# Kernel tuning notes

Measured on AMD Instinct MI355X. Metric: run time of the kernel, lower is better.

Reference implementation:

```python
import jax, jax.numpy as jnp
import numpy as np


def setup_inputs() -> dict:
    key = jax.random.key(0)
    ks = jax.random.split(key, 16)
    B, S, H = 512, 128, 256
    f32 = jnp.float32
    inputs = jax.random.normal(ks[0], (B, S, 2), f32)
    # xavier-normal-ish init (gain/sqrt(fan_in+fan_out) approximated by small scale)
    def xn(k, shape):
        fan = shape[0] + shape[1]
        return jax.random.normal(k, shape, f32) * np.sqrt(2.0 / fan)
    return {
        "inputs": inputs,
        "W0": xn(ks[1], (H, 2)),   "b0": jnp.zeros((H,), f32),
        "W1": xn(ks[2], (H, H)),   "b1": jnp.zeros((H,), f32),
        "W2": xn(ks[3], (H, H)),   "b2": jnp.zeros((H,), f32),
        "W3": xn(ks[4], (H, H)),   "b3": jnp.zeros((H,), f32),
        "W4": xn(ks[5], (1, H)),   "b4": jnp.zeros((1,), f32),
        "log_growth_rate": jax.random.normal(ks[6], (), f32),
        "log_carrying_capacity": jax.random.normal(ks[7], (), f32),
        "log_initial_loss": jax.random.normal(ks[8], (), f32),
        "in_mean": jnp.array([0.5, 50.0], f32),
        "in_std": jnp.array([0.2, 30.0], f32),
        "tgt_mean": jnp.array([0.8], f32),
        "tgt_std": jnp.array([0.1], f32),
    }


def reference(inputs, W0, b0, W1, b1, W2, b2, W3, b3, W4, b4,
              log_growth_rate, log_carrying_capacity, log_initial_loss,
              in_mean, in_std, tgt_mean, tgt_std):
    B, S = inputs.shape[0], inputs.shape[1]
    # PDE parameters (Verhulst logistic growth)
    r = jnp.exp(-log_growth_rate)
    K = 0.2 + (1.0 - 0.2) * jax.nn.sigmoid(log_carrying_capacity)  # carrying capacity in [0.2, 1]
    C = 0.0 + (0.1 - 0.0) * jax.nn.sigmoid(log_initial_loss)       # initial loss in [0, 0.1]

    # split state feature s and time t, standardize per-column
    s = inputs[..., 0:1].reshape(-1, 1)  # [N,1]
    t = inputs[..., 1:2].reshape(-1, 1)  # [N,1]
    s_norm = (s - in_mean[0:1]) / (in_std[0:1] + 1e-8)
    t_norm = (t - in_mean[1:2]) / (in_std[1:2] + 1e-8)

    Ws = (W0, W1, W2, W3, W4)
    bs = (b0, b1, b2, b3, b4)

    def mlp(x):  # [N,2] -> [N,1], tanh MLP
        h = x
        for W, b in zip(Ws[:-1], bs[:-1]):
            h = jnp.tanh(h @ W.T + b)
        return h @ Ws[-1].T + bs[-1]

    def u_of(tn):  # U(s_norm, tn), inverse-standardized targets
        return mlp(jnp.concatenate([s_norm, tn], axis=-1)) * tgt_std + tgt_mean

    ones = jnp.ones_like(t_norm)

    def uf_of(tn):
        # U and U_t = dU/dt_norm (forward-mode; each point depends on its own scalar t)
        U, U_dot = jax.jvp(u_of, (tn,), (ones,))
        U_t = U_dot.sum(-1, keepdims=True)
        G = r * (U - C) * (1.0 - (U - C) / (K - C))  # Verhulst
        return U, U_t - G  # (U, F)

    # second derivative w.r.t. t_norm: F_t = U_tt - G_t
    (U, F), (_, F_t) = jax.jvp(uf_of, (t_norm,), (ones,))

    shp = (B, S, 1)
    return U.reshape(shp), F.reshape(shp), F_t.reshape(shp)
```

## Files before the change

kernel.cpp:

```cpp
#include <hip/hip_runtime.h>
#include <hip/hip_bf16.h>
#include <math.h>

typedef short s8v __attribute__((ext_vector_type(8)));
typedef float f4v __attribute__((ext_vector_type(4)));

#define HH 256
#define TP 32
#define NTHREADS 256
#define KSTR 520
#define TSTR 4160
#define NTILES 6
#define PLANE (NTILES * TSTR)

__device__ __forceinline__ unsigned short bf_rne(float x){
    union{float f;unsigned u;}v; v.f=x;
    unsigned r = v.u + 0x7FFFu + ((v.u >> 16) & 1u);
    return (unsigned short)(r >> 16);
}
__device__ __forceinline__ unsigned pack_rne2(float a, float b){
    union { __hip_bfloat162 h; unsigned u; } v;
    v.h = __float22bfloat162_rn(float2{a, b});
    return v.u;
}

__global__ __launch_bounds__(256)
void prep_weights(const float* __restrict__ W1, const float* __restrict__ W2,
                  const float* __restrict__ W3, const float* __restrict__ W0,
                  const float* __restrict__ b0, const float* __restrict__ W4,
                  unsigned short* __restrict__ wsB, float* __restrict__ wsF)
{
    int t = blockIdx.x * 256 + threadIdx.x;
    if (t < 24576) {
        int layer = t >> 13;
        int rem = t & 8191;
        int l  = rem & 63;
        int ks = (rem >> 6) & 7;
        int nt = rem >> 9;
        const float* W = (layer == 0) ? W1 : (layer == 1) ? W2 : W3;
        int n_out = nt * 16 + (l & 15);
        int quad  = l >> 4;
        const float* row = W + n_out * HH;
        s8v hi;
        #pragma unroll
        for (int j = 0; j < 8; ++j) {
            int n_in = quad * 64 + (j & 3) * 16 + ((j >> 2) << 3) + ks;
            hi[j] = (short)bf_rne(row[n_in]);
        }
        int dst = ((nt * 8 + ks) * 64 + l) * 8;
        *(s8v*)(wsB + layer * 65536 + dst) = hi;
    } else if (t < 24832) {
        int n = t - 24576;
        int pos = ((n & 7) * 4 + (n >> 6)) * 8 + ((n >> 4) & 3) + 4 * ((n >> 3) & 1);
        wsF[pos]       = W0[2 * n];
        wsF[256 + pos] = W0[2 * n + 1];
        wsF[512 + pos] = b0[n];
        wsF[768 + pos] = W4[n];
    }
}

template<int H>
__device__ __forceinline__ void mfma_group(
    f4v (&acc)[3][4], const s8v (&Bv)[4][8],
    const unsigned short* Ahi, const float* __restrict__ bL,
    int lane, int w, int m16)
{
    #pragma unroll
    for (int i = 0; i < 4; ++i) {
        float bias = bL[w * 64 + i * 16 + m16];
        acc[0][i] = (f4v){bias, bias, bias, bias};
        acc[1][i] = (f4v){0.f, 0.f, 0.f, 0.f};
        acc[2][i] = (f4v){0.f, 0.f, 0.f, 0.f};
    }
    __builtin_amdgcn_s_setprio(1);
    #pragma unroll
    for (int ks = 0; ks < 8; ++ks) {
        const int aoff = ks * KSTR + lane * 8;
        s8v a0 = *(const s8v*)&Ahi[(0 + H) * TSTR + aoff];
        s8v a1 = *(const s8v*)&Ahi[(2 + H) * TSTR + aoff];
        s8v a2 = *(const s8v*)&Ahi[(4 + H) * TSTR + aoff];
        #pragma unroll
        for (int i = 0; i < 4; ++i) {
            acc[0][i] = __builtin_amdgcn_mfma_f32_16x16x32_bf16(a0, Bv[i][ks], acc[0][i], 0, 0, 0);
            acc[1][i] = __builtin_amdgcn_mfma_f32_16x16x32_bf16(a1, Bv[i][ks], acc[1][i], 0, 0, 0);
            acc[2][i] = __builtin_amdgcn_mfma_f32_16x16x32_bf16(a2, Bv[i][ks], acc[2][i], 0, 0, 0);
        }
    }
    __builtin_amdgcn_s_setprio(0);
}

template<int H>
__device__ __forceinline__ void transform_group(
    f4v (&acc)[3][4], unsigned short* Ahi, int w, int m16, int q)
{
    const int ksw  = m16 & 7;
    const int hsel = m16 >> 3;
    const int wbase = ksw * KSTR + (16 * w + q * 4) * 8 + 4 * hsel;
    #pragma unroll
    for (int r = 0; r < 4; ++r) {
        float Av[3][4];
        #pragma unroll
        for (int i = 0; i < 4; ++i) {
            float z  = acc[0][i][r];
            float z1 = acc[1][i][r];
            float z2 = acc[2][i][r];
            float e = __expf(2.f * z);
            float a = 1.f - 2.f * __builtin_amdgcn_rcpf(e + 1.f);
            float g = 1.f - a * a;
            float d1 = g * z1;
            float d2 = fmaf(g, z2, -2.f * a * d1 * z1);
            Av[0][i] = a; Av[1][i] = d1; Av[2][i] = d2;
        }
        #pragma unroll
        for (int s = 0; s < 3; ++s) {
            int2 hi2;
            hi2.x = (int)pack_rne2(Av[s][0], Av[s][1]);
            hi2.y = (int)pack_rne2(Av[s][2], Av[s][3]);
            *(int2*)&Ahi[(s * 2 + H) * TSTR + wbase + r * 8] = hi2;
        }
    }
}

template<int H>
__device__ __forceinline__ void head_group(
    f4v (&acc)[3][4], const float (&w4v)[4], float* head_part,
    int w, int m16, int q)
{
    float hp[3][4];
    #pragma unroll
    for (int s = 0; s < 3; ++s)
        #pragma unroll
        for (int r = 0; r < 4; ++r) hp[s][r] = 0.f;
    #pragma unroll
    for (int r = 0; r < 4; ++r) {
        #pragma unroll
        for (int i = 0; i < 4; ++i) {
            float z  = acc[0][i][r];
            float z1 = acc[1][i][r];
            float z2 = acc[2][i][r];
            float e = __expf(2.f * z);
            float a = 1.f - 2.f * __builtin_amdgcn_rcpf(e + 1.f);
            float g = 1.f - a * a;
            float d1 = g * z1;
            float d2 = fmaf(g, z2, -2.f * a * d1 * z1);
            hp[0][r] = fmaf(w4v[i], a,  hp[0][r]);
            hp[1][r] = fmaf(w4v[i], d1, hp[1][r]);
            hp[2][r] = fmaf(w4v[i], d2, hp[2][r]);
        }
    }
    #pragma unroll
    for (int m = 1; m < 16; m <<= 1) {
        #pragma unroll
        for (int s = 0; s < 3; ++s)
            #pragma unroll
            for (int r = 0; r < 4; ++r)
                hp[s][r] += __shfl_xor(hp[s][r], m);
    }
    if (m16 == 0) {
        #pragma unroll
        for (int s = 0; s < 3; ++s)
            #pragma unroll
            for (int r = 0; r < 4; ++r)
                head_part[(s * TP + H * 16 + q * 4 + r) * 4 + w] = hp[s][r];
    }
}

__global__ __launch_bounds__(NTHREADS, 2)
void capnn_mfma(const float* __restrict__ inp,
                const float* __restrict__ b1, const float* __restrict__ b2,
                const float* __restrict__ b3, const float* __restrict__ b4,
                const float* __restrict__ W4raw,
                const float* __restrict__ lgr, const float* __restrict__ lcc,
                const float* __restrict__ lil,
                const float* __restrict__ imean, const float* __restrict__ istd,
                const float* __restrict__ tmean, const float* __restrict__ tstd,
                const unsigned short* __restrict__ wsW,
                const float* __restrict__ wsF,
                float* __restrict__ out, int N)
{
    __shared__ __align__(16) unsigned short Ahi[PLANE];
    __shared__ float sn_sh[TP], tn_sh[TP];
    __shared__ float head_part[TP * 3 * 4];

    const int tid  = threadIdx.x;
    const int lane = tid & 63;
    const int w    = tid >> 6;
    const int m16  = lane & 15;
    const int q    = lane >> 4;
    const int pbase = blockIdx.x * TP;

    const float* __restrict__ w00p = wsF;
    const float* __restrict__ w01p = wsF + 256;
    const float* __restrict__ b0p  = wsF + 512;

    if (tid < TP) {
        int pg = pbase + tid;
        float s = 0.f, t = 0.f;
        if (pg < N) { s = inp[2 * pg]; t = inp[2 * pg + 1]; }
        sn_sh[tid] = (s - imean[0]) / (istd[0] + 1e-8f);
        tn_sh[tid] = (t - imean[1]) / (istd[1] + 1e-8f);
    }
    __syncthreads();

    {
        const int l  = lane;
        const int p16 = l & 15, quad = l >> 4;
        #pragma unroll
        for (int g2 = 0; g2 < 2; ++g2) {
            const int ks = w + 4 * g2;
            const int pos = (ks * 4 + quad) * 8;
            float4 wA0 = *(const float4*)(w00p + pos);
            float4 wA1 = *(const float4*)(w00p + pos + 4);
            float4 wB0 = *(const float4*)(w01p + pos);
            float4 wB1 = *(const float4*)(w01p + pos + 4);
            float4 bb0 = *(const float4*)(b0p + pos);
            float4 bb1 = *(const float4*)(b0p + pos + 4);
            float w00v[8] = {wA0.x,wA0.y,wA0.z,wA0.w,wA1.x,wA1.y,wA1.z,wA1.w};
            float w01v[8] = {wB0.x,wB0.y,wB0.z,wB0.w,wB1.x,wB1.y,wB1.z,wB1.w};
            float b0v[8]  = {bb0.x,bb0.y,bb0.z,bb0.w,bb1.x,bb1.y,bb1.z,bb1.w};
            const int base = ks * KSTR + l * 8;
            #pragma unroll
            for (int h = 0; h < 2; ++h) {
                const float sn = sn_sh[h * 16 + p16], tn = tn_sh[h * 16 + p16];
                float av[8], d1v[8], d2v[8];
                #pragma unroll
                for (int j = 0; j < 8; ++j) {
                    float z = fmaf(w00v[j], sn, fmaf(w01v[j], tn, b0v[j]));
                    float e = __expf(2.f * z);
                    float a = 1.f - 2.f * __builtin_amdgcn_rcpf(e + 1.f);
                    float g = 1.f - a * a;
                    float d1 = g * w01v[j];
                    float d2 = -2.f * a * d1 * w01v[j];
                    av[j] = a; d1v[j] = d1; d2v[j] = d2;
                }
                #pragma unroll
                for (int s = 0; s < 3; ++s) {
                    const float* V = (s == 0) ? av : (s == 1) ? d1v : d2v;
                    int4 hi4;
                    hi4.x = (int)pack_rne2(V[0], V[1]);
                    hi4.y = (int)pack_rne2(V[2], V[3]);
                    hi4.z = (int)pack_rne2(V[4], V[5]);
                    hi4.w = (int)pack_rne2(V[6], V[7]);
                    *(int4*)&Ahi[(s * 2 + h) * TSTR + base] = hi4;
                }
            }
        }
    }
    __syncthreads();

    f4v acc[3][4];

    #pragma unroll 1
    for (int L = 0; L < 2; ++L) {
        const unsigned short* __restrict__ Wlh = wsW + L * 65536;
        const float* __restrict__ bL = (L == 0) ? b1 : b2;

        s8v Bv[4][8];
        #pragma unroll
        for (int i = 0; i < 4; ++i)
            #pragma unroll
            for (int ks = 0; ks < 8; ++ks)
                Bv[i][ks] = *(const s8v*)(Wlh + (((w * 4 + i) * 8 + ks) * 64 + lane) * 8);

        mfma_group<0>(acc, Bv, Ahi, bL, lane, w, m16);
        __syncthreads();
        transform_group<0>(acc, Ahi, w, m16, q);
        mfma_group<1>(acc, Bv, Ahi, bL, lane, w, m16);
        __syncthreads();
        transform_group<1>(acc, Ahi, w, m16, q);
    }

    {
        const unsigned short* __restrict__ Wlh = wsW + 131072;
        s8v Bv[4][8];
        #pragma unroll
        for (int i = 0; i < 4; ++i)
            #pragma unroll
            for (int ks = 0; ks < 8; ++ks)
                Bv[i][ks] = *(const s8v*)(Wlh + (((w * 4 + i) * 8 + ks) * 64 + lane) * 8);

        float w4v[4];
        #pragma unroll
        for (int i = 0; i < 4; ++i) w4v[i] = W4raw[w * 64 + i * 16 + m16];

        mfma_group<0>(acc, Bv, Ahi, b3, lane, w, m16);
        head_group<0>(acc, w4v, head_part, w, m16, q);
        __syncthreads();
        mfma_group<1>(acc, Bv, Ahi, b3, lane, w, m16);
        head_group<1>(acc, w4v, head_part, w, m16, q);
    }
    __syncthreads();

    if (tid < TP) {
        float sv = 0.f, s1v = 0.f, s2v = 0.f;
        #pragma unroll
        for (int ww = 0; ww < 4; ++ww) {
            sv  += head_part[(0 * TP + tid) * 4 + ww];
            s1v += head_part[(1 * TP + tid) * 4 + ww];
            s2v += head_part[(2 * TP + tid) * 4 + ww];
        }
        int pg = pbase + tid;
        if (pg < N) {
            float r_  = expf(-lgr[0]);
            float Kc  = 0.2f + 0.8f / (1.f + expf(-lcc[0]));
            float Cc  = 0.1f / (1.f + expf(-lil[0]));
            float kci = 1.f / (Kc - Cc);
            float ts = tstd[0], tm = tmean[0];
            float U   = (sv + b4[0]) * ts + tm;
            float Ut  = s1v * ts;
            float Utt = s2v * ts;
            float Um  = U - Cc;
            float G   = r_ * Um * (1.f - Um * kci);
            float Gt  = r_ * Ut * (1.f - 2.f * Um * kci);
            out[pg]         = U;
            out[N + pg]     = Ut - G;
            out[2 * N + pg] = Utt - Gt;
        }
    }
}

extern "C" void kernel_launch(void* const* d_in, const int* in_sizes, int n_in,
                              void* d_out, int out_size, void* d_ws, size_t ws_size,
                              hipStream_t stream) {
    const float* inp   = (const float*)d_in[0];
    const float* W0    = (const float*)d_in[1];
    const float* b0    = (const float*)d_in[2];
    const float* W1    = (const float*)d_in[3];
    const float* b1    = (const float*)d_in[4];
    const float* W2    = (const float*)d_in[5];
    const float* b2    = (const float*)d_in[6];
    const float* W3    = (const float*)d_in[7];
    const float* b3    = (const float*)d_in[8];
    const float* W4    = (const float*)d_in[9];
    const float* b4    = (const float*)d_in[10];
    const float* lgr   = (const float*)d_in[11];
    const float* lcc   = (const float*)d_in[12];
    const float* lil   = (const float*)d_in[13];
    const float* imean = (const float*)d_in[14];
    const float* istd  = (const float*)d_in[15];
    const float* tmean = (const float*)d_in[16];
    const float* tstd  = (const float*)d_in[17];

    unsigned short* wsB = (unsigned short*)d_ws;
    float* wsF = (float*)((char*)d_ws + 393216);

    const int N = in_sizes[0] / 2;
    const int gridMain = (N + TP - 1) / TP;

    hipLaunchKernelGGL(prep_weights, dim3(97), dim3(256), 0, stream,
                       W1, W2, W3, W0, b0, W4, wsB, wsF);
    hipLaunchKernelGGL(capnn_mfma, dim3(gridMain), dim3(NTHREADS), 0, stream,
                       inp, b1, b2, b3, b4, W4,
                       lgr, lcc, lil, imean, istd, tmean, tstd,
                       wsB, wsF, (float*)d_out, N);
}
```

Before: 173.7 us.

## Double tile to 64 points per block and overlap MFMA with tanh transform

```diff
diff --git a/kernel.cpp b/kernel.cpp
--- a/kernel.cpp
+++ b/kernel.cpp
@@ -6,11 +6,12 @@
 typedef float f4v __attribute__((ext_vector_type(4)));
 
 #define HH 256
-#define TP 32
+#define TP 64
 #define NTHREADS 256
+#define NGRP 4
 #define KSTR 520
 #define TSTR 4160
-#define NTILES 6
+#define NTILES 12
 #define PLANE (NTILES * TSTR)
 
 __device__ __forceinline__ unsigned short bf_rne(float x){
@@ -76,9 +77,9 @@
     #pragma unroll
     for (int ks = 0; ks < 8; ++ks) {
         const int aoff = ks * KSTR + lane * 8;
-        s8v a0 = *(const s8v*)&Ahi[(0 + H) * TSTR + aoff];
-        s8v a1 = *(const s8v*)&Ahi[(2 + H) * TSTR + aoff];
-        s8v a2 = *(const s8v*)&Ahi[(4 + H) * TSTR + aoff];
+        s8v a0 = *(const s8v*)&Ahi[(0 * NGRP + H) * TSTR + aoff];
+        s8v a1 = *(const s8v*)&Ahi[(1 * NGRP + H) * TSTR + aoff];
+        s8v a2 = *(const s8v*)&Ahi[(2 * NGRP + H) * TSTR + aoff];
         #pragma unroll
         for (int i = 0; i < 4; ++i) {
             acc[0][i] = __builtin_amdgcn_mfma_f32_16x16x32_bf16(a0, Bv[i][ks], acc[0][i], 0, 0, 0);
@@ -116,7 +117,7 @@
             int2 hi2;
             hi2.x = (int)pack_rne2(Av[s][0], Av[s][1]);
             hi2.y = (int)pack_rne2(Av[s][2], Av[s][3]);
-            *(int2*)&Ahi[(s * 2 + H) * TSTR + wbase + r * 8] = hi2;
+            *(int2*)&Ahi[(s * NGRP + H) * TSTR + wbase + r * 8] = hi2;
         }
     }
 }
@@ -165,7 +166,17 @@
     }
 }
 
-__global__ __launch_bounds__(NTHREADS, 2)
+#define LOADB(Wlh)                                                          \
+    do {                                                                    \
+        _Pragma("unroll")                                                   \
+        for (int i = 0; i < 4; ++i)                                         \
+            _Pragma("unroll")                                               \
+            for (int ks = 0; ks < 8; ++ks)                                  \
+                Bv[i][ks] = *(const s8v*)((Wlh) +                           \
+                    (((w * 4 + i) * 8 + ks) * 64 + lane) * 8);              \
+    } while (0)
+
+__global__ __launch_bounds__(NTHREADS, 1)
 void capnn_mfma(const float* __restrict__ inp,
                 const float* __restrict__ b1, const float* __restrict__ b2,
                 const float* __restrict__ b3, const float* __restrict__ b4,
@@ -220,7 +231,7 @@
             float b0v[8]  = {bb0.x,bb0.y,bb0.z,bb0.w,bb1.x,bb1.y,bb1.z,bb1.w};
             const int base = ks * KSTR + l * 8;
             #pragma unroll
-            for (int h = 0; h < 2; ++h) {
+            for (int h = 0; h < NGRP; ++h) {
                 const float sn = sn_sh[h * 16 + p16], tn = tn_sh[h * 16 + p16];
                 float av[8], d1v[8], d2v[8];
                 #pragma unroll
@@ -241,54 +252,64 @@
                     hi4.y = (int)pack_rne2(V[2], V[3]);
                     hi4.z = (int)pack_rne2(V[4], V[5]);
                     hi4.w = (int)pack_rne2(V[6], V[7]);
-                    *(int4*)&Ahi[(s * 2 + h) * TSTR + base] = hi4;
+                    *(int4*)&Ahi[(s * NGRP + h) * TSTR + base] = hi4;
                 }
             }
         }
     }
     __syncthreads();
 
-    f4v acc[3][4];
-
-    #pragma unroll 1
-    for (int L = 0; L < 2; ++L) {
-        const unsigned short* __restrict__ Wlh = wsW + L * 65536;
-        const float* __restrict__ bL = (L == 0) ? b1 : b2;
-
-        s8v Bv[4][8];
-        #pragma unroll
-        for (int i = 0; i < 4; ++i)
-            #pragma unroll
-            for (int ks = 0; ks < 8; ++ks)
-                Bv[i][ks] = *(const s8v*)(Wlh + (((w * 4 + i) * 8 + ks) * 64 + lane) * 8);
-
-        mfma_group<0>(acc, Bv, Ahi, bL, lane, w, m16);
-        __syncthreads();
-        transform_group<0>(acc, Ahi, w, m16, q);
-        mfma_group<1>(acc, Bv, Ahi, bL, lane, w, m16);
-        __syncthreads();
-        transform_group<1>(acc, Ahi, w, m16, q);
-    }
-
-    {
-        const unsigned short* __restrict__ Wlh = wsW + 131072;
-        s8v Bv[4][8];
-        #pragma unroll
-        for (int i = 0; i < 4; ++i)
-            #pragma unroll
-            for (int ks = 0; ks < 8; ++ks)
-                Bv[i][ks] = *(const s8v*)(Wlh + (((w * 4 + i) * 8 + ks) * 64 + lane) * 8);
-
-        float w4v[4];
-        #pragma unroll
-        for (int i = 0; i < 4; ++i) w4v[i] = W4raw[w * 64 + i * 16 + m16];
-
-        mfma_group<0>(acc, Bv, Ahi, b3, lane, w, m16);
-        head_group<0>(acc, w4v, head_part, w, m16, q);
-        __syncthreads();
-        mfma_group<1>(acc, Bv, Ahi, b3, lane, w, m16);
-        head_group<1>(acc, w4v, head_part, w, m16, q);
-    }
+    f4v accA[3][4], accB[3][4];
+    s8v Bv[4][8];
+    const unsigned short* __restrict__ W1h = wsW;
+    const unsigned short* __restrict__ W2h = wsW + 65536;
+    const unsigned short* __restrict__ W3h = wsW + 131072;
+
+    LOADB(W1h);
+    mfma_group<0>(accA, Bv, Ahi, b1, lane, w, m16);
+    __syncthreads();
+    mfma_group<1>(accB, Bv, Ahi, b1, lane, w, m16);
+    transform_group<0>(accA, Ahi, w, m16, q);
+    __syncthreads();
+    mfma_group<2>(accA, Bv, Ahi, b1, lane, w, m16);
+    transform_group<1>(accB, Ahi, w, m16, q);
+    __syncthreads();
+    mfma_group<3>(accB, Bv, Ahi, b1, lane, w, m16);
+    transform_group<2>(accA, Ahi, w, m16, q);
+    __syncthreads();
+    transform_group<3>(accB, Ahi, w, m16, q);
+
+    LOADB(W2h);
+    mfma_group<0>(accA, Bv, Ahi, b2, lane, w, m16);
+    __syncthreads();
+    mfma_group<1>(accB, Bv, Ahi, b2, lane, w, m16);
+    transform_group<0>(accA, Ahi, w, m16, q);
+    __syncthreads();
+    mfma_group<2>(accA, Bv, Ahi, b2, lane, w, m16);
+    transform_group<1>(accB, Ahi, w, m16, q);
+    __syncthreads();
+    mfma_group<3>(accB, Bv, Ahi, b2, lane, w, m16);
+    transform_group<2>(accA, Ahi, w, m16, q);
+    __syncthreads();
+    transform_group<3>(accB, Ahi, w, m16, q);
+
+    LOADB(W3h);
+    float w4v[4];
+    #pragma unroll
+    for (int i = 0; i < 4; ++i) w4v[i] = W4raw[w * 64 + i * 16 + m16];
+
+    mfma_group<0>(accA, Bv, Ahi, b3, lane, w, m16);
+    __syncthreads();
+    mfma_group<1>(accB, Bv, Ahi, b3, lane, w, m16);
+    head_group<0>(accA, w4v, head_part, w, m16, q);
+    __syncthreads();
+    mfma_group<2>(accA, Bv, Ahi, b3, lane, w, m16);
+    head_group<1>(accB, w4v, head_part, w, m16, q);
+    __syncthreads();
+    mfma_group<3>(accB, Bv, Ahi, b3, lane, w, m16);
+    head_group<2>(accA, w4v, head_part, w, m16, q);
+    __syncthreads();
+    head_group<3>(accB, w4v, head_part, w, m16, q);
     __syncthreads();
 
     if (tid < TP) {
```

After: 196.7 us. 13.2% more time.
